# Kernel tuning notes

Hardware: AMD Instinct MI355X
Metric: run time of the kernel (lower is better)

## Reference

```python
import jax, jax.numpy as jnp
import numpy as np

N_HEADS = 4
TAU = 0.1
EPS = 1e-10


def positional_encoding(S, H, dtype):
    # standard sinusoidal PE, max_len >= S
    pos = jnp.arange(S, dtype=jnp.float32)[:, None]                      # [S,1]
    div = jnp.exp(jnp.arange(0, H, 2, dtype=jnp.float32) * (-np.log(10000.0) / H))
    pe = jnp.zeros((S, H), dtype=jnp.float32)
    pe = pe.at[:, 0::2].set(jnp.sin(pos * div))
    pe = pe.at[:, 1::2].set(jnp.cos(pos * div))
    return pe.astype(dtype)


def setup_inputs() -> dict:
    key = jax.random.key(0)
    k1, k2, k3, k4 = jax.random.split(key, 4)
    B, S, H, A, N = 1024, 100, 1024, 128, N_HEADS
    x = jax.random.normal(k1, (B, S, H), dtype=jnp.float32)
    Wq = jax.random.normal(k2, (A * N, H), dtype=jnp.float32) * (1.0 / np.sqrt(H))
    Wk = jax.random.normal(k3, (A * N, H), dtype=jnp.float32) * (1.0 / np.sqrt(H))
    gumbel_u = jax.random.uniform(k4, (B * N, S), dtype=jnp.float32)
    return {"x": x, "Wq": Wq, "Wk": Wk, "gumbel_u": gumbel_u}


def reference(x, Wq, Wk, gumbel_u):
    B, S, H = x.shape
    N = N_HEADS
    pe = x + positional_encoding(S, H, x.dtype)[None]                    # [B,S,H]
    # Q,K projections -> [B,N,S,A]
    Q = (pe @ Wq.T).reshape(B, S, N, -1).transpose(0, 2, 1, 3)
    K = (pe @ Wk.T).reshape(B, S, N, -1).transpose(0, 2, 1, 3)
    # sum_t (Q_s . K_t) == Q_s . sum_t(K_t): collapse O(S^2) score matrix to O(S)
    Ksum = K.sum(axis=2)                                                 # [B,N,A]
    logits = jnp.einsum('bnsa,bna->bns', Q, Ksum) / (jnp.sqrt(jnp.float32(H)) * S)
    logits = logits.reshape(B * N, S)
    # gumbel-softmax, hard=True (straight-through)
    g = -jnp.log(-jnp.log(gumbel_u + EPS) + EPS)
    y_soft = jax.nn.softmax((logits + g) / TAU, axis=-1)
    y_hard = jax.nn.one_hot(jnp.argmax(y_soft, axis=-1), S, dtype=y_soft.dtype)
    alphas = y_hard + y_soft - jax.lax.stop_gradient(y_soft)
    alphas = alphas.reshape(B, N, S)
    # weighted gather of the selected timestep(s)
    return jnp.einsum('bns,bsh->bnh', alphas, x)                         # [B,N,H]
```

## Files before the change

### kernel.cpp

```cpp
#include <hip/hip_runtime.h>
#include <hip/hip_bf16.h>
#include <math.h>

#define Bn 1024
#define Sn 100
#define Hn 1024
#define An 128
#define NHEADS 4
#define Jn 512

__global__ __launch_bounds__(256) void k0_pe(float* __restrict__ pe, float* __restrict__ pesum) {
    int h = blockIdx.x * 256 + threadIdx.x;
    if (h >= Hn) return;
    int i = h >> 1;
    const float c = (float)(-9.210340371976184 / (double)Hn);
    float divv = expf((float)(2 * i) * c);
    float sum = 0.f;
    for (int s = 0; s < Sn; ++s) {
        float arg = (float)s * divv;
        float val = (h & 1) ? cosf(arg) : sinf(arg);
        pe[(size_t)s * Hn + h] = val;
        sum += val;
    }
    pesum[h] = sum;
}

__global__ __launch_bounds__(256) void k1_xsum(const float* __restrict__ x,
                                               const float* __restrict__ pesum,
                                               float* __restrict__ xsum) {
    int b = blockIdx.x;
    int t = threadIdx.x;
    const float4* xp = (const float4*)(x + (size_t)b * Sn * Hn);
    float4 acc = ((const float4*)pesum)[t];
    #pragma unroll 4
    for (int s = 0; s < Sn; ++s) {
        float4 v = xp[(size_t)s * (Hn / 4) + t];
        acc.x += v.x; acc.y += v.y; acc.z += v.z; acc.w += v.w;
    }
    ((float4*)xsum)[(size_t)b * (Hn / 4) + t] = acc;
}

__global__ __launch_bounds__(256) void k2_gemm_abt(const float* __restrict__ Amat,
                                                   const float* __restrict__ Bmat,
                                                   float* __restrict__ Cmat) {
    __shared__ float As[16][36];
    __shared__ float Bs[16][68];
    int tid = threadIdx.x;
    int m0 = blockIdx.x * 32, j0 = blockIdx.y * 64;
    int tx = tid & 15, ty = tid >> 4;
    float acc[2][4] = {};
    int bj = tid >> 2, bk = (tid & 3) * 4;
    int am = tid >> 2, ak = (tid & 3) * 4;
    for (int kb = 0; kb < Hn; kb += 16) {
        float4 bv = *(const float4*)(Bmat + (size_t)(j0 + bj) * Hn + kb + bk);
        Bs[bk + 0][bj] = bv.x; Bs[bk + 1][bj] = bv.y; Bs[bk + 2][bj] = bv.z; Bs[bk + 3][bj] = bv.w;
        if (tid < 128) {
            float4 av = *(const float4*)(Amat + (size_t)(m0 + am) * Hn + kb + ak);
            As[ak + 0][am] = av.x; As[ak + 1][am] = av.y; As[ak + 2][am] = av.z; As[ak + 3][am] = av.w;
        }
        __syncthreads();
        #pragma unroll
        for (int kk = 0; kk < 16; ++kk) {
            float2 a = *(const float2*)&As[kk][ty * 2];
            float4 b = *(const float4*)&Bs[kk][tx * 4];
            acc[0][0] = fmaf(a.x, b.x, acc[0][0]);
            acc[0][1] = fmaf(a.x, b.y, acc[0][1]);
            acc[0][2] = fmaf(a.x, b.z, acc[0][2]);
            acc[0][3] = fmaf(a.x, b.w, acc[0][3]);
            acc[1][0] = fmaf(a.y, b.x, acc[1][0]);
            acc[1][1] = fmaf(a.y, b.y, acc[1][1]);
            acc[1][2] = fmaf(a.y, b.z, acc[1][2]);
            acc[1][3] = fmaf(a.y, b.w, acc[1][3]);
        }
        __syncthreads();
    }
    #pragma unroll
    for (int r = 0; r < 2; ++r) {
        float4 o = make_float4(acc[r][0], acc[r][1], acc[r][2], acc[r][3]);
        *(float4*)(Cmat + (size_t)(m0 + ty * 2 + r) * Jn + j0 + tx * 4) = o;
    }
}

__global__ __launch_bounds__(256) void k3_gemm_ab(const float* __restrict__ ksum,
                                                  const float* __restrict__ Wq,
                                                  float* __restrict__ v) {
    __shared__ float As[64][17];
    __shared__ float Bs[16][64];
    int tid = threadIdx.x;
    int m0 = blockIdx.x * 64, j0 = blockIdx.y * 64, n = blockIdx.z;
    int tx = tid & 15, ty = tid >> 4;
    float acc[4][4] = {};
    int li = tid * 4;
    int ar = li >> 4, ac = li & 15;
    int br = li >> 6, bc = li & 63;
    for (int kb = 0; kb < An; kb += 16) {
        float4 av = *(const float4*)(ksum + (size_t)(m0 + ar) * Jn + n * An + kb + ac);
        As[ar][ac + 0] = av.x; As[ar][ac + 1] = av.y; As[ar][ac + 2] = av.z; As[ar][ac + 3] = av.w;
        float4 bv = *(const float4*)(Wq + (size_t)(n * An + kb + br) * Hn + j0 + bc);
        Bs[br][bc + 0] = bv.x; Bs[br][bc + 1] = bv.y; Bs[br][bc + 2] = bv.z; Bs[br][bc + 3] = bv.w;
        __syncthreads();
        #pragma unroll
        for (int kk = 0; kk < 16; ++kk) {
            float a[4], b[4];
            #pragma unroll
            for (int r = 0; r < 4; ++r) a[r] = As[ty * 4 + r][kk];
            #pragma unroll
            for (int cidx = 0; cidx < 4; ++cidx) b[cidx] = Bs[kk][tx * 4 + cidx];
            #pragma unroll
            for (int r = 0; r < 4; ++r)
                #pragma unroll
                for (int cidx = 0; cidx < 4; ++cidx)
                    acc[r][cidx] = fmaf(a[r], b[cidx], acc[r][cidx]);
        }
        __syncthreads();
    }
    #pragma unroll
    for (int r = 0; r < 4; ++r) {
        int b = m0 + ty * 4 + r;
        #pragma unroll
        for (int cidx = 0; cidx < 4; ++cidx) {
            int h = j0 + tx * 4 + cidx;
            v[((size_t)b * NHEADS + n) * Hn + h] = acc[r][cidx];
        }
    }
}

__global__ __launch_bounds__(256) void k4_final(const float* __restrict__ x,
                                                const float* __restrict__ pe,
                                                const float* __restrict__ v,
                                                const float* __restrict__ gu,
                                                float* __restrict__ out) {
    int b = blockIdx.x;
    int tid = threadIdx.x;
    int wave = tid >> 6, lane = tid & 63;
    __shared__ float vL[NHEADS][Hn];
    __shared__ float redVal[4][NHEADS];
    __shared__ int redS[4][NHEADS];
    __shared__ int sstar[NHEADS];

    const float4* vg = (const float4*)(v + (size_t)b * NHEADS * Hn);
    float4* vls = (float4*)&vL[0][0];
    for (int i = tid; i < NHEADS * Hn / 4; i += 256) vls[i] = vg[i];
    __syncthreads();

    float bestVal[NHEADS] = {-1e30f, -1e30f, -1e30f, -1e30f};
    int bestS[NHEADS] = {0, 0, 0, 0};
    const float scale = 1.0f / 3200.0f;

    for (int s = wave; s < Sn; s += 4) {
        const float4* xr = (const float4*)(x + ((size_t)b * Sn + s) * Hn);
        const float4* pr = (const float4*)(pe + (size_t)s * Hn);
        float acc0 = 0.f, acc1 = 0.f, acc2 = 0.f, acc3 = 0.f;
        #pragma unroll
        for (int k = 0; k < 4; ++k) {
            int idx = k * 64 + lane;
            float4 xv = xr[idx];
            float4 pv = pr[idx];
            float t0 = xv.x + pv.x, t1 = xv.y + pv.y, t2 = xv.z + pv.z, t3 = xv.w + pv.w;
            float4 v0 = ((const float4*)&vL[0][0])[idx];
            float4 v1 = ((const float4*)&vL[1][0])[idx];
            float4 v2 = ((const float4*)&vL[2][0])[idx];
            float4 v3 = ((const float4*)&vL[3][0])[idx];
            acc0 += t0 * v0.x + t1 * v0.y + t2 * v0.z + t3 * v0.w;
            acc1 += t0 * v1.x + t1 * v1.y + t2 * v1.z + t3 * v1.w;
            acc2 += t0 * v2.x + t1 * v2.y + t2 * v2.z + t3 * v2.w;
            acc3 += t0 * v3.x + t1 * v3.y + t2 * v3.z + t3 * v3.w;
        }
        float accs[4] = {acc0, acc1, acc2, acc3};
        #pragma unroll
        for (int n = 0; n < NHEADS; ++n) {
            float a = accs[n];
            #pragma unroll
            for (int off = 32; off > 0; off >>= 1) a += __shfl_xor(a, off, 64);
            float u = gu[((size_t)b * NHEADS + n) * Sn + s];
            float g = -logf(-logf(u + 1e-10f) + 1e-10f);
            float tot = a * scale + g;
            if (tot > bestVal[n]) { bestVal[n] = tot; bestS[n] = s; }
        }
    }
    if (lane == 0) {
        #pragma unroll
        for (int n = 0; n < NHEADS; ++n) {
            redVal[wave][n] = bestVal[n];
            redS[wave][n] = bestS[n];
        }
    }
    __syncthreads();
    if (tid < NHEADS) {
        float bv = redVal[0][tid];
        int bs = redS[0][tid];
        for (int w = 1; w < 4; ++w) {
            float vv = redVal[w][tid];
            int ss = redS[w][tid];
            if (vv > bv || (vv == bv && ss < bs)) { bv = vv; bs = ss; }
        }
        sstar[tid] = bs;
    }
    __syncthreads();
    #pragma unroll
    for (int n = 0; n < NHEADS; ++n) {
        const float4* src = (const float4*)(x + ((size_t)b * Sn + sstar[n]) * Hn);
        float4* dst = (float4*)(out + ((size_t)b * NHEADS + n) * Hn);
        dst[tid] = src[tid];
    }
}

extern "C" void kernel_launch(void* const* d_in, const int* in_sizes, int n_in,
                              void* d_out, int out_size, void* d_ws, size_t ws_size,
                              hipStream_t stream) {
    const float* x  = (const float*)d_in[0];
    const float* Wq = (const float*)d_in[1];
    const float* Wk = (const float*)d_in[2];
    const float* gu = (const float*)d_in[3];
    float* out = (float*)d_out;
    float* ws = (float*)d_ws;

    float* pe    = ws;
    float* pesum = pe + (size_t)Sn * Hn;
    float* xsum  = pesum + Hn;
    float* ksum  = xsum + (size_t)Bn * Hn;
    float* v     = out;

    k0_pe<<<dim3(Hn / 256), dim3(256), 0, stream>>>(pe, pesum);
    k1_xsum<<<dim3(Bn), dim3(256), 0, stream>>>(x, pesum, xsum);
    k2_gemm_abt<<<dim3(Bn / 32, Jn / 64), dim3(256), 0, stream>>>(xsum, Wk, ksum);
    k3_gemm_ab<<<dim3(Bn / 64, Hn / 64, NHEADS), dim3(256), 0, stream>>>(ksum, Wq, v);
    k4_final<<<dim3(Bn), dim3(256), 0, stream>>>(x, pe, v, gu, out);
}
```

Measured before the change: 749.5 us.

## Parallelize PE generation, split-K larger-tile GEMMs, precompute gumbel noise in shared memory

The positional-encoding kernel now spreads work across one block per timestep, and a separate pass produces the column sums. Both GEMMs move to 128x128 tiles with an 8x8 register micro-tile per thread. The Wk GEMM is split along K into 8 partial slabs that a separate kernel adds together. The final kernel computes the gumbel noise once per block into shared memory instead of once per timestep per head. This raises arithmetic intensity and occupancy for the small GEMMs at the cost of extra launches, a partial-sum buffer in the workspace, and more register pressure.

```diff
diff --git a/kernel.cpp b/kernel.cpp
--- a/kernel.cpp
+++ b/kernel.cpp
@@ -8,21 +8,27 @@
 #define An 128
 #define NHEADS 4
 #define Jn 512
-
-__global__ __launch_bounds__(256) void k0_pe(float* __restrict__ pe, float* __restrict__ pesum) {
+#define KSPLIT 8
+
+__global__ __launch_bounds__(256) void k0a_pe(float* __restrict__ pe) {
+    int s = blockIdx.x;
+    int t = threadIdx.x;
+    int h0 = t * 4;
+    const float c = (float)(-9.210340371976184 / (double)Hn);
+    float d0 = expf((float)h0 * c);
+    float d1 = expf((float)(h0 + 2) * c);
+    float a0 = (float)s * d0, a1 = (float)s * d1;
+    float4 o;
+    o.x = sinf(a0); o.y = cosf(a0); o.z = sinf(a1); o.w = cosf(a1);
+    ((float4*)(pe + (size_t)s * Hn))[t] = o;
+}
+
+__global__ __launch_bounds__(256) void k0b_pesum(const float* __restrict__ pe,
+                                                 float* __restrict__ pesum) {
     int h = blockIdx.x * 256 + threadIdx.x;
-    if (h >= Hn) return;
-    int i = h >> 1;
-    const float c = (float)(-9.210340371976184 / (double)Hn);
-    float divv = expf((float)(2 * i) * c);
-    float sum = 0.f;
-    for (int s = 0; s < Sn; ++s) {
-        float arg = (float)s * divv;
-        float val = (h & 1) ? cosf(arg) : sinf(arg);
-        pe[(size_t)s * Hn + h] = val;
-        sum += val;
-    }
-    pesum[h] = sum;
+    float s = 0.f;
+    for (int i = 0; i < Sn; ++i) s += pe[(size_t)i * Hn + h];
+    pesum[h] = s;
 }
 
 __global__ __launch_bounds__(256) void k1_xsum(const float* __restrict__ x,
@@ -40,88 +46,111 @@
     ((float4*)xsum)[(size_t)b * (Hn / 4) + t] = acc;
 }
 
-__global__ __launch_bounds__(256) void k2_gemm_abt(const float* __restrict__ Amat,
-                                                   const float* __restrict__ Bmat,
-                                                   float* __restrict__ Cmat) {
-    __shared__ float As[16][36];
-    __shared__ float Bs[16][68];
+__global__ __launch_bounds__(256) void k2p_gemm(const float* __restrict__ Amat,
+                                                const float* __restrict__ Bmat,
+                                                float* __restrict__ kpart) {
+    __shared__ float Ast[16][132];
+    __shared__ float Bst[16][132];
     int tid = threadIdx.x;
-    int m0 = blockIdx.x * 32, j0 = blockIdx.y * 64;
+    int m0 = blockIdx.x * 128, j0 = blockIdx.y * 128;
+    int kc = blockIdx.z * 128;
     int tx = tid & 15, ty = tid >> 4;
-    float acc[2][4] = {};
-    int bj = tid >> 2, bk = (tid & 3) * 4;
-    int am = tid >> 2, ak = (tid & 3) * 4;
-    for (int kb = 0; kb < Hn; kb += 16) {
-        float4 bv = *(const float4*)(Bmat + (size_t)(j0 + bj) * Hn + kb + bk);
-        Bs[bk + 0][bj] = bv.x; Bs[bk + 1][bj] = bv.y; Bs[bk + 2][bj] = bv.z; Bs[bk + 3][bj] = bv.w;
-        if (tid < 128) {
-            float4 av = *(const float4*)(Amat + (size_t)(m0 + am) * Hn + kb + ak);
-            As[ak + 0][am] = av.x; As[ak + 1][am] = av.y; As[ak + 2][am] = av.z; As[ak + 3][am] = av.w;
-        }
+    int lr = tid >> 1, lc = (tid & 1) * 8;
+    float acc[8][8] = {};
+    for (int kb = 0; kb < 128; kb += 16) {
+        const float* ap = Amat + (size_t)(m0 + lr) * Hn + kc + kb + lc;
+        float4 a0v = *(const float4*)(ap), a1v = *(const float4*)(ap + 4);
+        Ast[lc + 0][lr] = a0v.x; Ast[lc + 1][lr] = a0v.y; Ast[lc + 2][lr] = a0v.z; Ast[lc + 3][lr] = a0v.w;
+        Ast[lc + 4][lr] = a1v.x; Ast[lc + 5][lr] = a1v.y; Ast[lc + 6][lr] = a1v.z; Ast[lc + 7][lr] = a1v.w;
+        const float* bp = Bmat + (size_t)(j0 + lr) * Hn + kc + kb + lc;
+        float4 b0v = *(const float4*)(bp), b1v = *(const float4*)(bp + 4);
+        Bst[lc + 0][lr] = b0v.x; Bst[lc + 1][lr] = b0v.y; Bst[lc + 2][lr] = b0v.z; Bst[lc + 3][lr] = b0v.w;
+        Bst[lc + 4][lr] = b1v.x; Bst[lc + 5][lr] = b1v.y; Bst[lc + 6][lr] = b1v.z; Bst[lc + 7][lr] = b1v.w;
         __syncthreads();
         #pragma unroll
         for (int kk = 0; kk < 16; ++kk) {
-            float2 a = *(const float2*)&As[kk][ty * 2];
-            float4 b = *(const float4*)&Bs[kk][tx * 4];
-            acc[0][0] = fmaf(a.x, b.x, acc[0][0]);
-            acc[0][1] = fmaf(a.x, b.y, acc[0][1]);
-            acc[0][2] = fmaf(a.x, b.z, acc[0][2]);
-            acc[0][3] = fmaf(a.x, b.w, acc[0][3]);
-            acc[1][0] = fmaf(a.y, b.x, acc[1][0]);
-            acc[1][1] = fmaf(a.y, b.y, acc[1][1]);
-            acc[1][2] = fmaf(a.y, b.z, acc[1][2]);
-            acc[1][3] = fmaf(a.y, b.w, acc[1][3]);
-        }
-        __syncthreads();
-    }
-    #pragma unroll
-    for (int r = 0; r < 2; ++r) {
-        float4 o = make_float4(acc[r][0], acc[r][1], acc[r][2], acc[r][3]);
-        *(float4*)(Cmat + (size_t)(m0 + ty * 2 + r) * Jn + j0 + tx * 4) = o;
-    }
-}
-
-__global__ __launch_bounds__(256) void k3_gemm_ab(const float* __restrict__ ksum,
-                                                  const float* __restrict__ Wq,
-                                                  float* __restrict__ v) {
-    __shared__ float As[64][17];
-    __shared__ float Bs[16][64];
+            float4 af0 = *(const float4*)&Ast[kk][ty * 8];
+            float4 af1 = *(const float4*)&Ast[kk][ty * 8 + 4];
+            float4 bf0 = *(const float4*)&Bst[kk][tx * 8];
+            float4 bf1 = *(const float4*)&Bst[kk][tx * 8 + 4];
+            float am[8] = {af0.x, af0.y, af0.z, af0.w, af1.x, af1.y, af1.z, af1.w};
+            float bn[8] = {bf0.x, bf0.y, bf0.z, bf0.w, bf1.x, bf1.y, bf1.z, bf1.w};
+            #pragma unroll
+            for (int r = 0; r < 8; ++r)
+                #pragma unroll
+                for (int cc = 0; cc < 8; ++cc)
+                    acc[r][cc] = fmaf(am[r], bn[cc], acc[r][cc]);
+        }
+        __syncthreads();
+    }
+    float* outp = kpart + (size_t)blockIdx.z * Bn * Jn;
+    #pragma unroll
+    for (int r = 0; r < 8; ++r) {
+        float4 o0 = make_float4(acc[r][0], acc[r][1], acc[r][2], acc[r][3]);
+        float4 o1 = make_float4(acc[r][4], acc[r][5], acc[r][6], acc[r][7]);
+        float* row = outp + (size_t)(m0 + ty * 8 + r) * Jn + j0 + tx * 8;
+        *(float4*)(row) = o0;
+        *(float4*)(row + 4) = o1;
+    }
+}
+
+__global__ __launch_bounds__(256) void k2r_reduce(const float* __restrict__ kpart,
+                                                  float* __restrict__ ksum) {
+    int i = blockIdx.x * 256 + threadIdx.x;
+    float4 s = ((const float4*)kpart)[i];
+    #pragma unroll
+    for (int sp = 1; sp < KSPLIT; ++sp) {
+        float4 p = ((const float4*)(kpart + (size_t)sp * Bn * Jn))[i];
+        s.x += p.x; s.y += p.y; s.z += p.z; s.w += p.w;
+    }
+    ((float4*)ksum)[i] = s;
+}
+
+__global__ __launch_bounds__(256) void k3p_gemm(const float* __restrict__ ksum,
+                                                const float* __restrict__ Wq,
+                                                float* __restrict__ v) {
+    __shared__ float Ast[16][132];
+    __shared__ float Bs[16][132];
     int tid = threadIdx.x;
-    int m0 = blockIdx.x * 64, j0 = blockIdx.y * 64, n = blockIdx.z;
+    int m0 = blockIdx.x * 128, h0 = blockIdx.y * 128, n = blockIdx.z;
     int tx = tid & 15, ty = tid >> 4;
-    float acc[4][4] = {};
-    int li = tid * 4;
-    int ar = li >> 4, ac = li & 15;
-    int br = li >> 6, bc = li & 63;
+    int lr = tid >> 1, lc = (tid & 1) * 8;
+    int brow = tid & 15, bseg = tid >> 4;
+    float acc[8][8] = {};
     for (int kb = 0; kb < An; kb += 16) {
-        float4 av = *(const float4*)(ksum + (size_t)(m0 + ar) * Jn + n * An + kb + ac);
-        As[ar][ac + 0] = av.x; As[ar][ac + 1] = av.y; As[ar][ac + 2] = av.z; As[ar][ac + 3] = av.w;
-        float4 bv = *(const float4*)(Wq + (size_t)(n * An + kb + br) * Hn + j0 + bc);
-        Bs[br][bc + 0] = bv.x; Bs[br][bc + 1] = bv.y; Bs[br][bc + 2] = bv.z; Bs[br][bc + 3] = bv.w;
+        const float* ap = ksum + (size_t)(m0 + lr) * Jn + n * An + kb + lc;
+        float4 a0v = *(const float4*)(ap), a1v = *(const float4*)(ap + 4);
+        Ast[lc + 0][lr] = a0v.x; Ast[lc + 1][lr] = a0v.y; Ast[lc + 2][lr] = a0v.z; Ast[lc + 3][lr] = a0v.w;
+        Ast[lc + 4][lr] = a1v.x; Ast[lc + 5][lr] = a1v.y; Ast[lc + 6][lr] = a1v.z; Ast[lc + 7][lr] = a1v.w;
+        const float* bp = Wq + (size_t)(n * An + kb + brow) * Hn + h0 + bseg * 8;
+        float4 w0 = *(const float4*)(bp), w1 = *(const float4*)(bp + 4);
+        *(float4*)&Bs[brow][bseg * 8] = w0;
+        *(float4*)&Bs[brow][bseg * 8 + 4] = w1;
         __syncthreads();
         #pragma unroll
         for (int kk = 0; kk < 16; ++kk) {
-            float a[4], b[4];
+            float4 af0 = *(const float4*)&Ast[kk][ty * 8];
+            float4 af1 = *(const float4*)&Ast[kk][ty * 8 + 4];
+            float4 bf0 = *(const float4*)&Bs[kk][tx * 8];
+            float4 bf1 = *(const float4*)&Bs[kk][tx * 8 + 4];
+            float am[8] = {af0.x, af0.y, af0.z, af0.w, af1.x, af1.y, af1.z, af1.w};
+            float bn[8] = {bf0.x, bf0.y, bf0.z, bf0.w, bf1.x, bf1.y, bf1.z, bf1.w};
             #pragma unroll
-            for (int r = 0; r < 4; ++r) a[r] = As[ty * 4 + r][kk];
-            #pragma unroll
-            for (int cidx = 0; cidx < 4; ++cidx) b[cidx] = Bs[kk][tx * 4 + cidx];
-            #pragma unroll
-            for (int r = 0; r < 4; ++r)
+            for (int r = 0; r < 8; ++r)
                 #pragma unroll
-                for (int cidx = 0; cidx < 4; ++cidx)
-                    acc[r][cidx] = fmaf(a[r], b[cidx], acc[r][cidx]);
-        }
-        __syncthreads();
-    }
-    #pragma unroll
-    for (int r = 0; r < 4; ++r) {
-        int b = m0 + ty * 4 + r;
-        #pragma unroll
-        for (int cidx = 0; cidx < 4; ++cidx) {
-            int h = j0 + tx * 4 + cidx;
-            v[((size_t)b * NHEADS + n) * Hn + h] = acc[r][cidx];
-        }
+                for (int cc = 0; cc < 8; ++cc)
+                    acc[r][cc] = fmaf(am[r], bn[cc], acc[r][cc]);
+        }
+        __syncthreads();
+    }
+    #pragma unroll
+    for (int r = 0; r < 8; ++r) {
+        int b = m0 + ty * 8 + r;
+        float* row = v + ((size_t)b * NHEADS + n) * Hn + h0 + tx * 8;
+        float4 o0 = make_float4(acc[r][0], acc[r][1], acc[r][2], acc[r][3]);
+        float4 o1 = make_float4(acc[r][4], acc[r][5], acc[r][6], acc[r][7]);
+        *(float4*)(row) = o0;
+        *(float4*)(row + 4) = o1;
     }
 }
 
@@ -134,6 +163,7 @@
     int tid = threadIdx.x;
     int wave = tid >> 6, lane = tid & 63;
     __shared__ float vL[NHEADS][Hn];
+    __shared__ float gL[NHEADS][Sn];
     __shared__ float redVal[4][NHEADS];
     __shared__ int redS[4][NHEADS];
     __shared__ int sstar[NHEADS];
@@ -141,6 +171,10 @@
     const float4* vg = (const float4*)(v + (size_t)b * NHEADS * Hn);
     float4* vls = (float4*)&vL[0][0];
     for (int i = tid; i < NHEADS * Hn / 4; i += 256) vls[i] = vg[i];
+    for (int i = tid; i < NHEADS * Sn; i += 256) {
+        float u = gu[(size_t)b * (NHEADS * Sn) + i];
+        gL[0][i] = -logf(-logf(u + 1e-10f) + 1e-10f);
+    }
     __syncthreads();
 
     float bestVal[NHEADS] = {-1e30f, -1e30f, -1e30f, -1e30f};
@@ -172,9 +206,7 @@
             float a = accs[n];
             #pragma unroll
             for (int off = 32; off > 0; off >>= 1) a += __shfl_xor(a, off, 64);
-            float u = gu[((size_t)b * NHEADS + n) * Sn + s];
-            float g = -logf(-logf(u + 1e-10f) + 1e-10f);
-            float tot = a * scale + g;
+            float tot = a * scale + gL[0][n * Sn + s];
             if (tot > bestVal[n]) { bestVal[n] = tot; bestS[n] = s; }
         }
     }
@@ -219,11 +251,14 @@
     float* pesum = pe + (size_t)Sn * Hn;
     float* xsum  = pesum + Hn;
     float* ksum  = xsum + (size_t)Bn * Hn;
+    float* kpart = ksum + (size_t)Bn * Jn;
     float* v     = out;
 
-    k0_pe<<<dim3(Hn / 256), dim3(256), 0, stream>>>(pe, pesum);
-    k1_xsum<<<dim3(Bn), dim3(256), 0, stream>>>(x, pesum, xsum);
-    k2_gemm_abt<<<dim3(Bn / 32, Jn / 64), dim3(256), 0, stream>>>(xsum, Wk, ksum);
-    k3_gemm_ab<<<dim3(Bn / 64, Hn / 64, NHEADS), dim3(256), 0, stream>>>(ksum, Wq, v);
-    k4_final<<<dim3(Bn), dim3(256), 0, stream>>>(x, pe, v, gu, out);
-}
+    k0a_pe   <<<dim3(Sn), dim3(256), 0, stream>>>(pe);
+    k0b_pesum<<<dim3(Hn / 256), dim3(256), 0, stream>>>(pe, pesum);
+    k1_xsum  <<<dim3(Bn), dim3(256), 0, stream>>>(x, pesum, xsum);
+    k2p_gemm <<<dim3(Bn / 128, Jn / 128, KSPLIT), dim3(256), 0, stream>>>(xsum, Wk, kpart);
+    k2r_reduce<<<dim3(Bn * Jn / 4 / 256), dim3(256), 0, stream>>>(kpart, ksum);
+    k3p_gemm <<<dim3(Bn / 128, Hn / 128, NHEADS), dim3(256), 0, stream>>>(ksum, Wq, v);
+    k4_final <<<dim3(Bn), dim3(256), 0, stream>>>(x, pe, v, gu, out);
+}
```

New measurement: 710.0 us. 5.3% less time.
